# Kernel tuning notes

Hardware: AMD Instinct MI355X
Metric: run time of the kernel (lower is better)

## Reference

```python
import jax, jax.numpy as jnp
import numpy as np

INTER = 32  # inter_channels = in_channels // 2


def conv1x1(x, w, b):
    # x: (b, c_in, h, w), w: (c_out, c_in), b: (c_out,)
    return jnp.einsum('bchw,oc->bohw', x, w) + b[None, :, None, None]


def setup_inputs() -> dict:
    key = jax.random.key(0)
    ks = jax.random.split(key, 12)
    B, C, H, W = 8, 64, 64, 64
    inter = INTER
    s_in = 1.0 / np.sqrt(C)      # torch conv default init scale
    s_int = 1.0 / np.sqrt(inter)
    return {
        'x': jax.random.normal(ks[0], (B, C, H, W), jnp.float32),
        'g_w': jax.random.normal(ks[1], (inter, C), jnp.float32) * s_in,
        'g_b': jax.random.normal(ks[2], (inter,), jnp.float32) * s_in,
        'theta_w': jax.random.normal(ks[3], (inter, C), jnp.float32) * s_in,
        'theta_b': jax.random.normal(ks[4], (inter,), jnp.float32) * s_in,
        'phi_w': jax.random.normal(ks[5], (inter, C), jnp.float32) * s_in,
        'phi_b': jax.random.normal(ks[6], (inter,), jnp.float32) * s_in,
        'W_w': jax.random.normal(ks[7], (C, inter), jnp.float32) * s_int,
        'W_b': jax.random.normal(ks[8], (C,), jnp.float32) * s_int,
        'Wz1_w': jax.random.normal(ks[9], (C, inter), jnp.float32) * s_int,
        'Wz1_b': jax.random.normal(ks[10], (C,), jnp.float32) * s_int,
        'mb': jax.random.normal(ks[11], (inter, 256), jnp.float32),
    }


def reference(x, g_w, g_b, theta_w, theta_b, phi_w, phi_b, W_w, W_b, Wz1_w, Wz1_b, mb):
    b, c, h, w = x.shape
    inter = g_w.shape[0]
    # 1x1 conv projections, flattened over spatial: N = h*w
    g_x = conv1x1(x, g_w, g_b).reshape(b, inter, -1)          # (b, ic, N)
    theta_x = conv1x1(x, theta_w, theta_b).reshape(b, inter, -1)
    phi_x = conv1x1(x, phi_w, phi_b).reshape(b, inter, -1)    # (b, ic, N)
    # non-local self-attention: f = theta^T @ phi, unscaled softmax
    f = jnp.einsum('bcn,bcm->bnm', theta_x, phi_x)            # (b, N, N)
    f_div_C = jax.nn.softmax(f, axis=-1)
    y = jnp.einsum('bnm,bcm->bcn', f_div_C, g_x)              # (b, ic, N)
    y = y.reshape(b, inter, h, w)
    W_y = conv1x1(y, W_w, W_b)                                # (b, c, h, w)
    # memory-bank cross-attention: phi^T @ mb, scaled softmax
    f1 = jnp.einsum('bcn,ck->bnk', phi_x, mb)                 # (b, N, 256)
    scale = jnp.float32(int(inter) ** (-0.5))
    f_div_C1 = jax.nn.softmax(f1 * scale, axis=-1)
    y1 = jnp.einsum('bnk,ck->bcn', f_div_C1, mb)              # (b, ic, N)
    y1 = y1.reshape(b, inter, h, w)
    W_y1 = conv1x1(y1, Wz1_w, Wz1_b)
    return W_y + x + W_y1
```

## Files before the change

kernel.cpp:

```cpp
#include <hip/hip_runtime.h>
#include <hip/hip_bf16.h>

#define N_POS 4096
#define C_IN 64
#define IC 32
#define L2E 1.4426950408889634f

typedef float f32x16 __attribute__((ext_vector_type(16)));
typedef short bf16x8 __attribute__((ext_vector_type(8)));
typedef unsigned int uint;
typedef uint uint4v __attribute__((ext_vector_type(4)));
typedef unsigned short ushort;

static __device__ __forceinline__ ushort f2bf(float f) {
    __hip_bfloat16 h = __float2bfloat16(f);
    return __builtin_bit_cast(ushort, h);
}
static __device__ __forceinline__ float bf2f(ushort u) {
    uint v = ((uint)u) << 16;
    return __builtin_bit_cast(float, v);
}
static __device__ __forceinline__ uint packbf2(float lo, float hi) {
    return (uint)f2bf(lo) | ((uint)f2bf(hi) << 16);
}
static __device__ __forceinline__ uint packtrunc(float lo, float hi) {
    return __builtin_amdgcn_perm(__builtin_bit_cast(uint, hi),
                                 __builtin_bit_cast(uint, lo), 0x07060302u);
}

__global__ __launch_bounds__(128) void proj_kernel(
    const float* __restrict__ x,
    const float* __restrict__ g_w, const float* __restrict__ g_b,
    const float* __restrict__ th_w, const float* __restrict__ th_b,
    const float* __restrict__ ph_w, const float* __restrict__ ph_b,
    const float* __restrict__ mb,
    ushort* __restrict__ gcn, ushort* __restrict__ tht, ushort* __restrict__ pht,
    ushort* __restrict__ mbt, ushort* __restrict__ mbb)
{
    int gy = blockIdx.y;
    int pj = gy >> 1, half = gy & 1;
    const float* wsrc = (pj == 0) ? g_w : (pj == 1) ? th_w : ph_w;
    const float* bsrc = (pj == 0) ? g_b : (pj == 1) ? th_b : ph_b;
    __shared__ float w[16][64];
    __shared__ float bias[16];
    int tid = threadIdx.x;
    for (int i = tid; i < 1024; i += 128) w[i >> 6][i & 63] = wsrc[half * 1024 + i];
    if (tid < 16) bias[tid] = bsrc[half * 16 + tid];
    __syncthreads();

    int ng = blockIdx.x * 128 + tid;
    int b = ng >> 12, n = ng & 4095;
    const float* xb = x + (size_t)b * C_IN * N_POS + n;
    float xr[64];
    #pragma unroll
    for (int c = 0; c < 64; c++) xr[c] = xb[(size_t)c * N_POS];

    float acc[16];
    #pragma unroll
    for (int o = 0; o < 16; o++) {
        float a = bias[o];
        const float4* w4 = (const float4*)w[o];
        #pragma unroll
        for (int c4 = 0; c4 < 16; c4++) {
            float4 wv = w4[c4];
            a += wv.x * xr[c4*4+0] + wv.y * xr[c4*4+1]
               + wv.z * xr[c4*4+2] + wv.w * xr[c4*4+3];
        }
        if (pj == 1) a *= L2E;
        acc[o] = a;
    }

    if (pj == 0) {
        #pragma unroll
        for (int c = 0; c < 16; c++)
            gcn[((size_t)(b * IC + half * 16 + c)) * N_POS + n] = f2bf(acc[c]);
    } else {
        ushort* dst = ((pj == 1) ? tht : pht) + ((size_t)(b * N_POS + n)) * IC + half * 16;
        uint4v pk0, pk1;
        #pragma unroll
        for (int i = 0; i < 4; i++) pk0[i] = packbf2(acc[2*i], acc[2*i+1]);
        #pragma unroll
        for (int i = 0; i < 4; i++) pk1[i] = packbf2(acc[8+2*i], acc[8+2*i+1]);
        *(uint4v*)dst = pk0;
        *(uint4v*)(dst + 8) = pk1;
    }

    if (gy == 0 && blockIdx.x < 64) {
        int i = blockIdx.x * 128 + tid;
        int c = i >> 8, k = i & 255;
        float v = mb[i];
        mbb[i] = f2bf(v);
        mbt[k * 32 + c] = f2bf(v * (0.17677669529663687f * L2E));
    }
}

__global__ __launch_bounds__(256) void attn_kernel(
    const ushort* __restrict__ tht, const ushort* __restrict__ pht,
    const ushort* __restrict__ gcn, float* __restrict__ yp,
    float* __restrict__ dnm)
{
    __shared__ float redY[4][2][32][32];
    __shared__ float redD[4][2][32];
    int tid = threadIdx.x;
    int s = tid >> 6, lane = tid & 63;
    int bid = blockIdx.x;
    int b = bid & 7;
    int rest = bid >> 3;
    int qp = rest >> 1;
    int half = rest & 1;
    int q0 = qp * 64;
    int mbase = (half * 4 + s) * 512;
    int cl = lane & 31, h = lane >> 5;
    int t4 = (cl >> 2) & 3;
    int pcl = (t4 == 1 || t4 == 2) ? (cl ^ 12) : cl;

    const ushort* thpA = tht + ((size_t)(b * N_POS + q0 + cl)) * IC + 8 * h;
    bf16x8 thA0 = *(const bf16x8*)thpA;
    bf16x8 thA1 = *(const bf16x8*)(thpA + 16);
    const ushort* thpB = thpA + 32 * IC;
    bf16x8 thB0 = *(const bf16x8*)thpB;
    bf16x8 thB1 = *(const bf16x8*)(thpB + 16);

    const ushort* phbase = pht + (size_t)b * N_POS * IC;
    const ushort* gbase  = gcn + ((size_t)(b * IC + cl)) * N_POS;

    f32x16 yA0, yA1, yB0, yB1, zero;
    #pragma unroll
    for (int i = 0; i < 16; i++) {
        yA0[i] = 0.f; yA1[i] = 0.f; yB0[i] = 0.f; yB1[i] = 0.f; zero[i] = 0.f;
    }
    float sumeA = 0.f, sumeB = 0.f;

    #pragma unroll 2
    for (int mt = 0; mt < 16; ++mt) {
        int m0 = mbase + mt * 32;
        const ushort* php = phbase + ((size_t)(m0 + pcl)) * IC + 8 * h;
        bf16x8 ph0 = *(const bf16x8*)php;
        bf16x8 ph1 = *(const bf16x8*)(php + 16);
        const ushort* gp = gbase + m0 + 8 * h;
        bf16x8 g0 = *(const bf16x8*)gp;
        bf16x8 g1 = *(const bf16x8*)(gp + 16);

        f32x16 sv = __builtin_amdgcn_mfma_f32_32x32x16_bf16(ph0, thA0, zero, 0, 0, 0);
        sv = __builtin_amdgcn_mfma_f32_32x32x16_bf16(ph1, thA1, sv, 0, 0, 0);
        uint wA[8];
        #pragma unroll
        for (int i = 0; i < 8; i++) {
            float p0 = __builtin_amdgcn_exp2f(sv[2*i]);
            float p1 = __builtin_amdgcn_exp2f(sv[2*i+1]);
            sumeA += p0 + p1;
            wA[i] = packtrunc(p0, p1);
        }
        f32x16 sw = __builtin_amdgcn_mfma_f32_32x32x16_bf16(ph0, thB0, zero, 0, 0, 0);
        sw = __builtin_amdgcn_mfma_f32_32x32x16_bf16(ph1, thB1, sw, 0, 0, 0);
        uint wB[8];
        #pragma unroll
        for (int i = 0; i < 8; i++) {
            float p0 = __builtin_amdgcn_exp2f(sw[2*i]);
            float p1 = __builtin_amdgcn_exp2f(sw[2*i+1]);
            sumeB += p0 + p1;
            wB[i] = packtrunc(p0, p1);
        }

        uint4v aA0, aA1, aB0, aB1;
        aA0[0] = wA[0]; aA0[1] = wA[1]; aA0[2] = wA[2]; aA0[3] = wA[3];
        aA1[0] = wA[4]; aA1[1] = wA[5]; aA1[2] = wA[6]; aA1[3] = wA[7];
        aB0[0] = wB[0]; aB0[1] = wB[1]; aB0[2] = wB[2]; aB0[3] = wB[3];
        aB1[0] = wB[4]; aB1[1] = wB[5]; aB1[2] = wB[6]; aB1[3] = wB[7];

        yA0 = __builtin_amdgcn_mfma_f32_32x32x16_bf16(
            __builtin_bit_cast(bf16x8, aA0), g0, yA0, 0, 0, 0);
        yA1 = __builtin_amdgcn_mfma_f32_32x32x16_bf16(
            __builtin_bit_cast(bf16x8, aA1), g1, yA1, 0, 0, 0);
        yB0 = __builtin_amdgcn_mfma_f32_32x32x16_bf16(
            __builtin_bit_cast(bf16x8, aB0), g0, yB0, 0, 0, 0);
        yB1 = __builtin_amdgcn_mfma_f32_32x32x16_bf16(
            __builtin_bit_cast(bf16x8, aB1), g1, yB1, 0, 0, 0);
    }

    sumeA += __shfl_xor(sumeA, 32);
    sumeB += __shfl_xor(sumeB, 32);
    if (lane < 32) { redD[s][0][cl] = sumeA; redD[s][1][cl] = sumeB; }
    #pragma unroll
    for (int r = 0; r < 16; r++) {
        int q = (r & 3) + 8 * (r >> 2) + 4 * h;
        redY[s][0][q][cl] = yA0[r] + yA1[r];
        redY[s][1][q][cl] = yB0[r] + yB1[r];
    }
    __syncthreads();

    int q = tid >> 3, c4 = tid & 7;
    #pragma unroll
    for (int j = 0; j < 2; j++) {
        float den = redD[0][j][q] + redD[1][j][q] + redD[2][j][q] + redD[3][j][q];
        float4 v0 = *(const float4*)&redY[0][j][q][c4 * 4];
        float4 v1 = *(const float4*)&redY[1][j][q][c4 * 4];
        float4 v2 = *(const float4*)&redY[2][j][q][c4 * 4];
        float4 v3 = *(const float4*)&redY[3][j][q][c4 * 4];
        float4 vv;
        vv.x = v0.x + v1.x + v2.x + v3.x;
        vv.y = v0.y + v1.y + v2.y + v3.y;
        vv.z = v0.z + v1.z + v2.z + v3.z;
        vv.w = v0.w + v1.w + v2.w + v3.w;
        size_t t = ((size_t)(b * 128 + qp * 2 + j)) * 2 + half;
        *(float4*)(yp + t * 1024 + q * 32 + c4 * 4) = vv;
        if (c4 == 0) dnm[t * 32 + q] = den;
    }
}

__global__ __launch_bounds__(256) void mbout_kernel(
    const ushort* __restrict__ pht, const ushort* __restrict__ mbt,
    const ushort* __restrict__ mbb, const float* __restrict__ yp,
    const float* __restrict__ dnm, const float* __restrict__ x,
    const float* __restrict__ Ww, const float* __restrict__ Wb,
    const float* __restrict__ Wzw, const float* __restrict__ Wzb,
    float* __restrict__ out)
{
    __shared__ float sW[64][32], sWz[64][32];
    __shared__ float sb[64];
    __shared__ float ly1p[4][32][36];
    __shared__ float sumeL[4][32];
    int tid = threadIdx.x;
    int bid = blockIdx.x;
    int b = bid & 7, grp = bid >> 3;
    int n0 = grp * 64;

    for (int i = tid; i < 2048; i += 256) {
        sW[i >> 5][i & 31]  = Ww[i];
        sWz[i >> 5][i & 31] = Wzw[i];
    }
    if (tid < 64) sb[tid] = Wb[tid] + Wzb[tid];

    int s = tid >> 6, lane = tid & 63;
    int j = s & 1, kh = s >> 1;
    int q0 = n0 + j * 32;
    int cl = lane & 31, h = lane >> 5;
    int t4 = (cl >> 2) & 3;
    int pcl = (t4 == 1 || t4 == 2) ? (cl ^ 12) : cl;

    const ushort* php = pht + ((size_t)(b * N_POS + q0 + cl)) * IC + 8 * h;
    bf16x8 qf0 = *(const bf16x8*)php;
    bf16x8 qf1 = *(const bf16x8*)(php + 16);

    f32x16 yaccA, yaccB, zero;
    #pragma unroll
    for (int i = 0; i < 16; i++) { yaccA[i] = 0.f; yaccB[i] = 0.f; zero[i] = 0.f; }
    float sume = 0.f;

    #pragma unroll
    for (int kt = 0; kt < 4; ++kt) {
        int k0 = (kh * 4 + kt) * 32;
        const ushort* ap = mbt + ((size_t)(k0 + pcl)) * IC + 8 * h;
        bf16x8 af0 = *(const bf16x8*)ap;
        bf16x8 af1 = *(const bf16x8*)(ap + 16);
        const ushort* bp = mbb + (size_t)cl * 256 + k0 + 8 * h;
        bf16x8 bf0 = *(const bf16x8*)bp;
        bf16x8 bf1 = *(const bf16x8*)(bp + 16);

        f32x16 sv = __builtin_amdgcn_mfma_f32_32x32x16_bf16(af0, qf0, zero, 0, 0, 0);
        sv = __builtin_amdgcn_mfma_f32_32x32x16_bf16(af1, qf1, sv, 0, 0, 0);

        uint w[8];
        #pragma unroll
        for (int i = 0; i < 8; i++) {
            float p0 = __builtin_amdgcn_exp2f(sv[2*i]);
            float p1 = __builtin_amdgcn_exp2f(sv[2*i+1]);
            sume += p0 + p1;
            w[i] = packtrunc(p0, p1);
        }
        uint4v a0, a1;
        a0[0] = w[0]; a0[1] = w[1]; a0[2] = w[2]; a0[3] = w[3];
        a1[0] = w[4]; a1[1] = w[5]; a1[2] = w[6]; a1[3] = w[7];

        yaccA = __builtin_amdgcn_mfma_f32_32x32x16_bf16(
            __builtin_bit_cast(bf16x8, a0), bf0, yaccA, 0, 0, 0);
        yaccB = __builtin_amdgcn_mfma_f32_32x32x16_bf16(
            __builtin_bit_cast(bf16x8, a1), bf1, yaccB, 0, 0, 0);
    }

    sume += __shfl_xor(sume, 32);
    if (lane < 32) sumeL[s][cl] = sume;
    #pragma unroll
    for (int r = 0; r < 16; r++) {
        int q = (r & 3) + 8 * (r >> 2) + 4 * h;
        ly1p[s][q][cl] = yaccA[r] + yaccB[r];
    }
    __syncthreads();

    int obase = (s & 1) * 32 + (s >> 1) * 16;
    int n = n0 + lane;
    int jj = lane >> 5, q = lane & 31;

    float inv1 = 1.f / (sumeL[jj][q] + sumeL[2 + jj][q]);
    float y1v[32];
    #pragma unroll
    for (int c4 = 0; c4 < 8; c4++) {
        float4 p0 = *(const float4*)&ly1p[jj][q][c4 * 4];
        float4 p1 = *(const float4*)&ly1p[2 + jj][q][c4 * 4];
        y1v[c4*4+0] = (p0.x + p1.x) * inv1;
        y1v[c4*4+1] = (p0.y + p1.y) * inv1;
        y1v[c4*4+2] = (p0.z + p1.z) * inv1;
        y1v[c4*4+3] = (p0.w + p1.w) * inv1;
    }

    int qt = n >> 5;
    size_t t0 = ((size_t)(b * 128 + qt)) * 2;
    float inv = 1.f / (dnm[t0 * 32 + q] + dnm[t0 * 32 + 32 + q]);
    const float* yp0 = yp + t0 * 1024 + q * 32;
    const float* yp1 = yp0 + 1024;
    float yv[32];
    #pragma unroll
    for (int c4 = 0; c4 < 8; c4++) {
        float4 v0 = ((const float4*)yp0)[c4];
        float4 v1 = ((const float4*)yp1)[c4];
        yv[c4*4+0] = (v0.x + v1.x) * inv;
        yv[c4*4+1] = (v0.y + v1.y) * inv;
        yv[c4*4+2] = (v0.z + v1.z) * inv;
        yv[c4*4+3] = (v0.w + v1.w) * inv;
    }

    const float* xb = x   + ((size_t)(b * C_IN + obase)) * N_POS + n;
    float*       ob = out + ((size_t)(b * C_IN + obase)) * N_POS + n;
    for (int o = 0; o < 16; o++) {
        float acc = sb[obase + o] + xb[(size_t)o * N_POS];
        const float4* w4  = (const float4*)sW[obase + o];
        const float4* wz4 = (const float4*)sWz[obase + o];
        #pragma unroll
        for (int c4 = 0; c4 < 8; c4++) {
            float4 a = w4[c4], z = wz4[c4];
            acc += a.x * yv[c4*4+0] + a.y * yv[c4*4+1] + a.z * yv[c4*4+2] + a.w * yv[c4*4+3];
            acc += z.x * y1v[c4*4+0] + z.y * y1v[c4*4+1] + z.z * y1v[c4*4+2] + z.w * y1v[c4*4+3];
        }
        ob[(size_t)o * N_POS] = acc;
    }
}

extern "C" void kernel_launch(void* const* d_in, const int* in_sizes, int n_in,
                              void* d_out, int out_size, void* d_ws, size_t ws_size,
                              hipStream_t stream) {
    const float* x    = (const float*)d_in[0];
    const float* g_w  = (const float*)d_in[1];
    const float* g_b  = (const float*)d_in[2];
    const float* th_w = (const float*)d_in[3];
    const float* th_b = (const float*)d_in[4];
    const float* ph_w = (const float*)d_in[5];
    const float* ph_b = (const float*)d_in[6];
    const float* W_w  = (const float*)d_in[7];
    const float* W_b  = (const float*)d_in[8];
    const float* Wz_w = (const float*)d_in[9];
    const float* Wz_b = (const float*)d_in[10];
    const float* mb   = (const float*)d_in[11];
    float* out = (float*)d_out;

    char* w = (char*)d_ws;
    ushort* tht = (ushort*)w;
    ushort* pht = (ushort*)(w + (2u << 20));
    ushort* gcn = (ushort*)(w + (4u << 20));
    ushort* mbt = (ushort*)(w + (6u << 20));
    ushort* mbb = (ushort*)(w + (6u << 20) + 16384);
    float*  yp  = (float*)(w + (9u << 20));
    float*  dnm = (float*)(w + (17u << 20));

    proj_kernel<<<dim3(256, 6), 128, 0, stream>>>(x, g_w, g_b, th_w, th_b,
                                                  ph_w, ph_b, mb,
                                                  gcn, tht, pht, mbt, mbb);
    attn_kernel<<<1024, 256, 0, stream>>>(tht, pht, gcn, yp, dnm);
    mbout_kernel<<<512, 256, 0, stream>>>(pht, mbt, mbb, yp, dnm, x,
                                          W_w, W_b, Wz_w, Wz_b, out);
}
```

Baseline: 78.07 us.

## Fuse attention, memory-bank attention and output projection into one kernel

The separate attention and memory-bank/output kernels are merged into one 512-thread kernel. Each block now covers all 4096 keys for 64 queries using 8 waves, instead of two half-key blocks that wrote partial sums to global memory. After the attention loop, four waves compute the memory-bank attention while the other four add their partial outputs in shared memory. This removes the yp/dnm global round trip and one kernel launch. The cost is only 512 blocks with bigger blocks and more registers, and output weights are now read straight from global memory instead of being staged in shared memory.

```diff
diff --git a/kernel.cpp b/kernel.cpp
--- a/kernel.cpp
+++ b/kernel.cpp
@@ -15,10 +15,6 @@
 static __device__ __forceinline__ ushort f2bf(float f) {
     __hip_bfloat16 h = __float2bfloat16(f);
     return __builtin_bit_cast(ushort, h);
-}
-static __device__ __forceinline__ float bf2f(ushort u) {
-    uint v = ((uint)u) << 16;
-    return __builtin_bit_cast(float, v);
 }
 static __device__ __forceinline__ uint packbf2(float lo, float hi) {
     return (uint)f2bf(lo) | ((uint)f2bf(hi) << 16);
@@ -94,22 +90,26 @@
     }
 }
 
-__global__ __launch_bounds__(256) void attn_kernel(
+__global__ __launch_bounds__(512) void attn_fused(
     const ushort* __restrict__ tht, const ushort* __restrict__ pht,
-    const ushort* __restrict__ gcn, float* __restrict__ yp,
-    float* __restrict__ dnm)
+    const ushort* __restrict__ gcn, const ushort* __restrict__ mbt,
+    const ushort* __restrict__ mbb, const float* __restrict__ x,
+    const float* __restrict__ Ww, const float* __restrict__ Wb,
+    const float* __restrict__ Wzw, const float* __restrict__ Wzb,
+    float* __restrict__ out)
 {
-    __shared__ float redY[4][2][32][32];
-    __shared__ float redD[4][2][32];
+    __shared__ float redY[4][2][32][36];
+    __shared__ float redD[8][2][32];
+    __shared__ float ly1p[4][32][36];
+    __shared__ float sumeL[4][32];
+
     int tid = threadIdx.x;
     int s = tid >> 6, lane = tid & 63;
     int bid = blockIdx.x;
     int b = bid & 7;
-    int rest = bid >> 3;
-    int qp = rest >> 1;
-    int half = rest & 1;
+    int qp = bid >> 3;
     int q0 = qp * 64;
-    int mbase = (half * 4 + s) * 512;
+    int mbase = s * 512;
     int cl = lane & 31, h = lane >> 5;
     int t4 = (cl >> 2) & 3;
     int pcl = (t4 == 1 || t4 == 2) ? (cl ^ 12) : cl;
@@ -181,150 +181,114 @@
     sumeA += __shfl_xor(sumeA, 32);
     sumeB += __shfl_xor(sumeB, 32);
     if (lane < 32) { redD[s][0][cl] = sumeA; redD[s][1][cl] = sumeB; }
-    #pragma unroll
-    for (int r = 0; r < 16; r++) {
-        int q = (r & 3) + 8 * (r >> 2) + 4 * h;
-        redY[s][0][q][cl] = yA0[r] + yA1[r];
-        redY[s][1][q][cl] = yB0[r] + yB1[r];
+    if (s < 4) {
+        #pragma unroll
+        for (int r = 0; r < 16; r++) {
+            int q = (r & 3) + 8 * (r >> 2) + 4 * h;
+            redY[s][0][q][cl] = yA0[r] + yA1[r];
+            redY[s][1][q][cl] = yB0[r] + yB1[r];
+        }
     }
     __syncthreads();
 
-    int q = tid >> 3, c4 = tid & 7;
-    #pragma unroll
-    for (int j = 0; j < 2; j++) {
-        float den = redD[0][j][q] + redD[1][j][q] + redD[2][j][q] + redD[3][j][q];
-        float4 v0 = *(const float4*)&redY[0][j][q][c4 * 4];
-        float4 v1 = *(const float4*)&redY[1][j][q][c4 * 4];
-        float4 v2 = *(const float4*)&redY[2][j][q][c4 * 4];
-        float4 v3 = *(const float4*)&redY[3][j][q][c4 * 4];
-        float4 vv;
-        vv.x = v0.x + v1.x + v2.x + v3.x;
-        vv.y = v0.y + v1.y + v2.y + v3.y;
-        vv.z = v0.z + v1.z + v2.z + v3.z;
-        vv.w = v0.w + v1.w + v2.w + v3.w;
-        size_t t = ((size_t)(b * 128 + qp * 2 + j)) * 2 + half;
-        *(float4*)(yp + t * 1024 + q * 32 + c4 * 4) = vv;
-        if (c4 == 0) dnm[t * 32 + q] = den;
-    }
-}
-
-__global__ __launch_bounds__(256) void mbout_kernel(
-    const ushort* __restrict__ pht, const ushort* __restrict__ mbt,
-    const ushort* __restrict__ mbb, const float* __restrict__ yp,
-    const float* __restrict__ dnm, const float* __restrict__ x,
-    const float* __restrict__ Ww, const float* __restrict__ Wb,
-    const float* __restrict__ Wzw, const float* __restrict__ Wzb,
-    float* __restrict__ out)
-{
-    __shared__ float sW[64][32], sWz[64][32];
-    __shared__ float sb[64];
-    __shared__ float ly1p[4][32][36];
-    __shared__ float sumeL[4][32];
-    int tid = threadIdx.x;
-    int bid = blockIdx.x;
-    int b = bid & 7, grp = bid >> 3;
-    int n0 = grp * 64;
-
-    for (int i = tid; i < 2048; i += 256) {
-        sW[i >> 5][i & 31]  = Ww[i];
-        sWz[i >> 5][i & 31] = Wzw[i];
-    }
-    if (tid < 64) sb[tid] = Wb[tid] + Wzb[tid];
-
-    int s = tid >> 6, lane = tid & 63;
-    int j = s & 1, kh = s >> 1;
-    int q0 = n0 + j * 32;
-    int cl = lane & 31, h = lane >> 5;
-    int t4 = (cl >> 2) & 3;
-    int pcl = (t4 == 1 || t4 == 2) ? (cl ^ 12) : cl;
-
-    const ushort* php = pht + ((size_t)(b * N_POS + q0 + cl)) * IC + 8 * h;
-    bf16x8 qf0 = *(const bf16x8*)php;
-    bf16x8 qf1 = *(const bf16x8*)(php + 16);
-
-    f32x16 yaccA, yaccB, zero;
-    #pragma unroll
-    for (int i = 0; i < 16; i++) { yaccA[i] = 0.f; yaccB[i] = 0.f; zero[i] = 0.f; }
-    float sume = 0.f;
-
-    #pragma unroll
-    for (int kt = 0; kt < 4; ++kt) {
-        int k0 = (kh * 4 + kt) * 32;
-        const ushort* ap = mbt + ((size_t)(k0 + pcl)) * IC + 8 * h;
-        bf16x8 af0 = *(const bf16x8*)ap;
-        bf16x8 af1 = *(const bf16x8*)(ap + 16);
-        const ushort* bp = mbb + (size_t)cl * 256 + k0 + 8 * h;
-        bf16x8 bf0 = *(const bf16x8*)bp;
-        bf16x8 bf1 = *(const bf16x8*)(bp + 16);
-
-        f32x16 sv = __builtin_amdgcn_mfma_f32_32x32x16_bf16(af0, qf0, zero, 0, 0, 0);
-        sv = __builtin_amdgcn_mfma_f32_32x32x16_bf16(af1, qf1, sv, 0, 0, 0);
-
-        uint w[8];
-        #pragma unroll
-        for (int i = 0; i < 8; i++) {
-            float p0 = __builtin_amdgcn_exp2f(sv[2*i]);
-            float p1 = __builtin_amdgcn_exp2f(sv[2*i+1]);
-            sume += p0 + p1;
-            w[i] = packtrunc(p0, p1);
-        }
-        uint4v a0, a1;
-        a0[0] = w[0]; a0[1] = w[1]; a0[2] = w[2]; a0[3] = w[3];
-        a1[0] = w[4]; a1[1] = w[5]; a1[2] = w[6]; a1[3] = w[7];
-
-        yaccA = __builtin_amdgcn_mfma_f32_32x32x16_bf16(
-            __builtin_bit_cast(bf16x8, a0), bf0, yaccA, 0, 0, 0);
-        yaccB = __builtin_amdgcn_mfma_f32_32x32x16_bf16(
-            __builtin_bit_cast(bf16x8, a1), bf1, yaccB, 0, 0, 0);
-    }
-
-    sume += __shfl_xor(sume, 32);
-    if (lane < 32) sumeL[s][cl] = sume;
-    #pragma unroll
-    for (int r = 0; r < 16; r++) {
-        int q = (r & 3) + 8 * (r >> 2) + 4 * h;
-        ly1p[s][q][cl] = yaccA[r] + yaccB[r];
+    if (s >= 4) {
+        int sl = s - 4;
+        #pragma unroll
+        for (int r = 0; r < 16; r++) {
+            int q = (r & 3) + 8 * (r >> 2) + 4 * h;
+            redY[sl][0][q][cl] += yA0[r] + yA1[r];
+            redY[sl][1][q][cl] += yB0[r] + yB1[r];
+        }
+    } else {
+        int j = s & 1, kh = s >> 1;
+        int mq0 = q0 + j * 32;
+        const ushort* php = pht + ((size_t)(b * N_POS + mq0 + cl)) * IC + 8 * h;
+        bf16x8 qf0 = *(const bf16x8*)php;
+        bf16x8 qf1 = *(const bf16x8*)(php + 16);
+
+        f32x16 zA, zB;
+        #pragma unroll
+        for (int i = 0; i < 16; i++) { zA[i] = 0.f; zB[i] = 0.f; }
+        float sume = 0.f;
+
+        #pragma unroll
+        for (int kt = 0; kt < 4; ++kt) {
+            int k0 = (kh * 4 + kt) * 32;
+            const ushort* ap = mbt + ((size_t)(k0 + pcl)) * IC + 8 * h;
+            bf16x8 af0 = *(const bf16x8*)ap;
+            bf16x8 af1 = *(const bf16x8*)(ap + 16);
+            const ushort* bp = mbb + (size_t)cl * 256 + k0 + 8 * h;
+            bf16x8 bf0 = *(const bf16x8*)bp;
+            bf16x8 bf1 = *(const bf16x8*)(bp + 16);
+
+            f32x16 sv = __builtin_amdgcn_mfma_f32_32x32x16_bf16(af0, qf0, zero, 0, 0, 0);
+            sv = __builtin_amdgcn_mfma_f32_32x32x16_bf16(af1, qf1, sv, 0, 0, 0);
+
+            uint w[8];
+            #pragma unroll
+            for (int i = 0; i < 8; i++) {
+                float p0 = __builtin_amdgcn_exp2f(sv[2*i]);
+                float p1 = __builtin_amdgcn_exp2f(sv[2*i+1]);
+                sume += p0 + p1;
+                w[i] = packtrunc(p0, p1);
+            }
+            uint4v a0, a1;
+            a0[0] = w[0]; a0[1] = w[1]; a0[2] = w[2]; a0[3] = w[3];
+            a1[0] = w[4]; a1[1] = w[5]; a1[2] = w[6]; a1[3] = w[7];
+
+            zA = __builtin_amdgcn_mfma_f32_32x32x16_bf16(
+                __builtin_bit_cast(bf16x8, a0), bf0, zA, 0, 0, 0);
+            zB = __builtin_amdgcn_mfma_f32_32x32x16_bf16(
+                __builtin_bit_cast(bf16x8, a1), bf1, zB, 0, 0, 0);
+        }
+
+        sume += __shfl_xor(sume, 32);
+        if (lane < 32) sumeL[s][cl] = sume;
+        #pragma unroll
+        for (int r = 0; r < 16; r++) {
+            int q = (r & 3) + 8 * (r >> 2) + 4 * h;
+            ly1p[s][q][cl] = zA[r] + zB[r];
+        }
     }
     __syncthreads();
 
-    int obase = (s & 1) * 32 + (s >> 1) * 16;
-    int n = n0 + lane;
-    int jj = lane >> 5, q = lane & 31;
-
-    float inv1 = 1.f / (sumeL[jj][q] + sumeL[2 + jj][q]);
-    float y1v[32];
+    int nl = lane, og = s;
+    int n = q0 + nl;
+    int jo = nl >> 5, qo = nl & 31;
+
+    float den = 0.f;
+    #pragma unroll
+    for (int s8 = 0; s8 < 8; s8++) den += redD[s8][jo][qo];
+    float inv = 1.f / den;
+    float inv1 = 1.f / (sumeL[jo][qo] + sumeL[2 + jo][qo]);
+
+    float yv[32], y1v[32];
     #pragma unroll
     for (int c4 = 0; c4 < 8; c4++) {
-        float4 p0 = *(const float4*)&ly1p[jj][q][c4 * 4];
-        float4 p1 = *(const float4*)&ly1p[2 + jj][q][c4 * 4];
+        float4 v0 = *(const float4*)&redY[0][jo][qo][c4 * 4];
+        float4 v1 = *(const float4*)&redY[1][jo][qo][c4 * 4];
+        float4 v2 = *(const float4*)&redY[2][jo][qo][c4 * 4];
+        float4 v3 = *(const float4*)&redY[3][jo][qo][c4 * 4];
+        yv[c4*4+0] = (v0.x + v1.x + v2.x + v3.x) * inv;
+        yv[c4*4+1] = (v0.y + v1.y + v2.y + v3.y) * inv;
+        yv[c4*4+2] = (v0.z + v1.z + v2.z + v3.z) * inv;
+        yv[c4*4+3] = (v0.w + v1.w + v2.w + v3.w) * inv;
+        float4 p0 = *(const float4*)&ly1p[jo][qo][c4 * 4];
+        float4 p1 = *(const float4*)&ly1p[2 + jo][qo][c4 * 4];
         y1v[c4*4+0] = (p0.x + p1.x) * inv1;
         y1v[c4*4+1] = (p0.y + p1.y) * inv1;
         y1v[c4*4+2] = (p0.z + p1.z) * inv1;
         y1v[c4*4+3] = (p0.w + p1.w) * inv1;
     }
 
-    int qt = n >> 5;
-    size_t t0 = ((size_t)(b * 128 + qt)) * 2;
-    float inv = 1.f / (dnm[t0 * 32 + q] + dnm[t0 * 32 + 32 + q]);
-    const float* yp0 = yp + t0 * 1024 + q * 32;
-    const float* yp1 = yp0 + 1024;
-    float yv[32];
-    #pragma unroll
-    for (int c4 = 0; c4 < 8; c4++) {
-        float4 v0 = ((const float4*)yp0)[c4];
-        float4 v1 = ((const float4*)yp1)[c4];
-        yv[c4*4+0] = (v0.x + v1.x) * inv;
-        yv[c4*4+1] = (v0.y + v1.y) * inv;
-        yv[c4*4+2] = (v0.z + v1.z) * inv;
-        yv[c4*4+3] = (v0.w + v1.w) * inv;
-    }
-
+    int obase = og * 8;
     const float* xb = x   + ((size_t)(b * C_IN + obase)) * N_POS + n;
     float*       ob = out + ((size_t)(b * C_IN + obase)) * N_POS + n;
-    for (int o = 0; o < 16; o++) {
-        float acc = sb[obase + o] + xb[(size_t)o * N_POS];
-        const float4* w4  = (const float4*)sW[obase + o];
-        const float4* wz4 = (const float4*)sWz[obase + o];
+    #pragma unroll
+    for (int o = 0; o < 8; o++) {
+        float acc = Wb[obase + o] + Wzb[obase + o] + xb[(size_t)o * N_POS];
+        const float4* w4  = (const float4*)(Ww  + (obase + o) * 32);
+        const float4* wz4 = (const float4*)(Wzw + (obase + o) * 32);
         #pragma unroll
         for (int c4 = 0; c4 < 8; c4++) {
             float4 a = w4[c4], z = wz4[c4];
@@ -358,13 +322,10 @@
     ushort* gcn = (ushort*)(w + (4u << 20));
     ushort* mbt = (ushort*)(w + (6u << 20));
     ushort* mbb = (ushort*)(w + (6u << 20) + 16384);
-    float*  yp  = (float*)(w + (9u << 20));
-    float*  dnm = (float*)(w + (17u << 20));
 
     proj_kernel<<<dim3(256, 6), 128, 0, stream>>>(x, g_w, g_b, th_w, th_b,
                                                   ph_w, ph_b, mb,
                                                   gcn, tht, pht, mbt, mbb);
-    attn_kernel<<<1024, 256, 0, stream>>>(tht, pht, gcn, yp, dnm);
-    mbout_kernel<<<512, 256, 0, stream>>>(pht, mbt, mbb, yp, dnm, x,
-                                          W_w, W_b, Wz_w, Wz_b, out);
-}
+    attn_fused<<<512, 512, 0, stream>>>(tht, pht, gcn, mbt, mbb, x,
+                                        W_w, W_b, Wz_w, Wz_b, out);
+}
```

After: 74.31 us. -4.8%, faster.

## Widen attention query tile to 128 and split projection into quarter-channel blocks

Applied to the files above, without the earlier changes.

The attention kernel now gives each block 128 queries (four 32-row tiles) instead of 64. Each loaded phi/g tile is reused across four query tiles, and the grid drops to 512 blocks. The cross-wave reduction now goes through a padded shared buffer with two-stage accumulation, and the partial-sum layout in yp/dnm changes to match, with the consumer kernel updated accordingly. Separately, the projection kernel is split into 12 y-blocks of 8 output channels each, raising parallelism at the cost of re-reading x more times. The wider tile raises register pressure (four accumulators plus eight theta fragments) and halves the number of attention blocks, which may hurt occupancy.

```diff
diff --git a/kernel.cpp b/kernel.cpp
--- a/kernel.cpp
+++ b/kernel.cpp
@@ -15,10 +15,6 @@
 static __device__ __forceinline__ ushort f2bf(float f) {
     __hip_bfloat16 h = __float2bfloat16(f);
     return __builtin_bit_cast(ushort, h);
-}
-static __device__ __forceinline__ float bf2f(ushort u) {
-    uint v = ((uint)u) << 16;
-    return __builtin_bit_cast(float, v);
 }
 static __device__ __forceinline__ uint packbf2(float lo, float hi) {
     return (uint)f2bf(lo) | ((uint)f2bf(hi) << 16);
@@ -38,14 +34,14 @@
     ushort* __restrict__ mbt, ushort* __restrict__ mbb)
 {
     int gy = blockIdx.y;
-    int pj = gy >> 1, half = gy & 1;
+    int pj = gy >> 2, q8 = gy & 3;
     const float* wsrc = (pj == 0) ? g_w : (pj == 1) ? th_w : ph_w;
     const float* bsrc = (pj == 0) ? g_b : (pj == 1) ? th_b : ph_b;
-    __shared__ float w[16][64];
-    __shared__ float bias[16];
+    __shared__ float w[8][64];
+    __shared__ float bias[8];
     int tid = threadIdx.x;
-    for (int i = tid; i < 1024; i += 128) w[i >> 6][i & 63] = wsrc[half * 1024 + i];
-    if (tid < 16) bias[tid] = bsrc[half * 16 + tid];
+    for (int i = tid; i < 512; i += 128) w[i >> 6][i & 63] = wsrc[q8 * 512 + i];
+    if (tid < 8) bias[tid] = bsrc[q8 * 8 + tid];
     __syncthreads();
 
     int ng = blockIdx.x * 128 + tid;
@@ -55,9 +51,9 @@
     #pragma unroll
     for (int c = 0; c < 64; c++) xr[c] = xb[(size_t)c * N_POS];
 
-    float acc[16];
-    #pragma unroll
-    for (int o = 0; o < 16; o++) {
+    float acc[8];
+    #pragma unroll
+    for (int o = 0; o < 8; o++) {
         float a = bias[o];
         const float4* w4 = (const float4*)w[o];
         #pragma unroll
@@ -72,17 +68,14 @@
 
     if (pj == 0) {
         #pragma unroll
-        for (int c = 0; c < 16; c++)
-            gcn[((size_t)(b * IC + half * 16 + c)) * N_POS + n] = f2bf(acc[c]);
+        for (int c = 0; c < 8; c++)
+            gcn[((size_t)(b * IC + q8 * 8 + c)) * N_POS + n] = f2bf(acc[c]);
     } else {
-        ushort* dst = ((pj == 1) ? tht : pht) + ((size_t)(b * N_POS + n)) * IC + half * 16;
-        uint4v pk0, pk1;
-        #pragma unroll
-        for (int i = 0; i < 4; i++) pk0[i] = packbf2(acc[2*i], acc[2*i+1]);
-        #pragma unroll
-        for (int i = 0; i < 4; i++) pk1[i] = packbf2(acc[8+2*i], acc[8+2*i+1]);
-        *(uint4v*)dst = pk0;
-        *(uint4v*)(dst + 8) = pk1;
+        ushort* dst = ((pj == 1) ? tht : pht) + ((size_t)(b * N_POS + n)) * IC + q8 * 8;
+        uint4v pk;
+        #pragma unroll
+        for (int i = 0; i < 4; i++) pk[i] = packbf2(acc[2*i], acc[2*i+1]);
+        *(uint4v*)dst = pk;
     }
 
     if (gy == 0 && blockIdx.x < 64) {
@@ -99,37 +92,60 @@
     const ushort* __restrict__ gcn, float* __restrict__ yp,
     float* __restrict__ dnm)
 {
-    __shared__ float redY[4][2][32][32];
-    __shared__ float redD[4][2][32];
+    __shared__ float redY[2][4][32][36];
+    __shared__ float redD[4][4][32];
     int tid = threadIdx.x;
     int s = tid >> 6, lane = tid & 63;
     int bid = blockIdx.x;
     int b = bid & 7;
     int rest = bid >> 3;
-    int qp = rest >> 1;
-    int half = rest & 1;
-    int q0 = qp * 64;
-    int mbase = (half * 4 + s) * 512;
+    int qq = rest >> 1;
+    int mh = rest & 1;
+    int q0 = qq * 128;
+    int mbase = (mh * 4 + s) * 512;
     int cl = lane & 31, h = lane >> 5;
     int t4 = (cl >> 2) & 3;
     int pcl = (t4 == 1 || t4 == 2) ? (cl ^ 12) : cl;
 
-    const ushort* thpA = tht + ((size_t)(b * N_POS + q0 + cl)) * IC + 8 * h;
-    bf16x8 thA0 = *(const bf16x8*)thpA;
-    bf16x8 thA1 = *(const bf16x8*)(thpA + 16);
-    const ushort* thpB = thpA + 32 * IC;
-    bf16x8 thB0 = *(const bf16x8*)thpB;
-    bf16x8 thB1 = *(const bf16x8*)(thpB + 16);
+    const ushort* thp = tht + ((size_t)(b * N_POS + q0 + cl)) * IC + 8 * h;
+    bf16x8 th00 = *(const bf16x8*)thp;
+    bf16x8 th01 = *(const bf16x8*)(thp + 16);
+    bf16x8 th10 = *(const bf16x8*)(thp + 32 * IC);
+    bf16x8 th11 = *(const bf16x8*)(thp + 32 * IC + 16);
+    bf16x8 th20 = *(const bf16x8*)(thp + 64 * IC);
+    bf16x8 th21 = *(const bf16x8*)(thp + 64 * IC + 16);
+    bf16x8 th30 = *(const bf16x8*)(thp + 96 * IC);
+    bf16x8 th31 = *(const bf16x8*)(thp + 96 * IC + 16);
 
     const ushort* phbase = pht + (size_t)b * N_POS * IC;
     const ushort* gbase  = gcn + ((size_t)(b * IC + cl)) * N_POS;
 
-    f32x16 yA0, yA1, yB0, yB1, zero;
+    f32x16 y0, y1a, y2, y3, zero;
     #pragma unroll
     for (int i = 0; i < 16; i++) {
-        yA0[i] = 0.f; yA1[i] = 0.f; yB0[i] = 0.f; yB1[i] = 0.f; zero[i] = 0.f;
-    }
-    float sumeA = 0.f, sumeB = 0.f;
+        y0[i] = 0.f; y1a[i] = 0.f; y2[i] = 0.f; y3[i] = 0.f; zero[i] = 0.f;
+    }
+    float su0 = 0.f, su1 = 0.f, su2 = 0.f, su3 = 0.f;
+
+#define QTILE(T0, T1, SU, Y) do {                                              \
+        f32x16 sv = __builtin_amdgcn_mfma_f32_32x32x16_bf16(ph0, T0, zero, 0, 0, 0); \
+        sv = __builtin_amdgcn_mfma_f32_32x32x16_bf16(ph1, T1, sv, 0, 0, 0);    \
+        uint w_[8];                                                            \
+        _Pragma("unroll")                                                      \
+        for (int i_ = 0; i_ < 8; i_++) {                                       \
+            float p0_ = __builtin_amdgcn_exp2f(sv[2*i_]);                      \
+            float p1_ = __builtin_amdgcn_exp2f(sv[2*i_+1]);                    \
+            SU += p0_ + p1_;                                                   \
+            w_[i_] = packtrunc(p0_, p1_);                                      \
+        }                                                                      \
+        uint4v a0_, a1_;                                                       \
+        a0_[0] = w_[0]; a0_[1] = w_[1]; a0_[2] = w_[2]; a0_[3] = w_[3];        \
+        a1_[0] = w_[4]; a1_[1] = w_[5]; a1_[2] = w_[6]; a1_[3] = w_[7];        \
+        Y = __builtin_amdgcn_mfma_f32_32x32x16_bf16(                           \
+            __builtin_bit_cast(bf16x8, a0_), g0, Y, 0, 0, 0);                  \
+        Y = __builtin_amdgcn_mfma_f32_32x32x16_bf16(                           \
+            __builtin_bit_cast(bf16x8, a1_), g1, Y, 0, 0, 0);                  \
+    } while (0)
 
     #pragma unroll 2
     for (int mt = 0; mt < 16; ++mt) {
@@ -141,70 +157,55 @@
         bf16x8 g0 = *(const bf16x8*)gp;
         bf16x8 g1 = *(const bf16x8*)(gp + 16);
 
-        f32x16 sv = __builtin_amdgcn_mfma_f32_32x32x16_bf16(ph0, thA0, zero, 0, 0, 0);
-        sv = __builtin_amdgcn_mfma_f32_32x32x16_bf16(ph1, thA1, sv, 0, 0, 0);
-        uint wA[8];
-        #pragma unroll
-        for (int i = 0; i < 8; i++) {
-            float p0 = __builtin_amdgcn_exp2f(sv[2*i]);
-            float p1 = __builtin_amdgcn_exp2f(sv[2*i+1]);
-            sumeA += p0 + p1;
-            wA[i] = packtrunc(p0, p1);
-        }
-        f32x16 sw = __builtin_amdgcn_mfma_f32_32x32x16_bf16(ph0, thB0, zero, 0, 0, 0);
-        sw = __builtin_amdgcn_mfma_f32_32x32x16_bf16(ph1, thB1, sw, 0, 0, 0);
-        uint wB[8];
-        #pragma unroll
-        for (int i = 0; i < 8; i++) {
-            float p0 = __builtin_amdgcn_exp2f(sw[2*i]);
-            float p1 = __builtin_amdgcn_exp2f(sw[2*i+1]);
-            sumeB += p0 + p1;
-            wB[i] = packtrunc(p0, p1);
-        }
-
-        uint4v aA0, aA1, aB0, aB1;
-        aA0[0] = wA[0]; aA0[1] = wA[1]; aA0[2] = wA[2]; aA0[3] = wA[3];
-        aA1[0] = wA[4]; aA1[1] = wA[5]; aA1[2] = wA[6]; aA1[3] = wA[7];
-        aB0[0] = wB[0]; aB0[1] = wB[1]; aB0[2] = wB[2]; aB0[3] = wB[3];
-        aB1[0] = wB[4]; aB1[1] = wB[5]; aB1[2] = wB[6]; aB1[3] = wB[7];
-
-        yA0 = __builtin_amdgcn_mfma_f32_32x32x16_bf16(
-            __builtin_bit_cast(bf16x8, aA0), g0, yA0, 0, 0, 0);
-        yA1 = __builtin_amdgcn_mfma_f32_32x32x16_bf16(
-            __builtin_bit_cast(bf16x8, aA1), g1, yA1, 0, 0, 0);
-        yB0 = __builtin_amdgcn_mfma_f32_32x32x16_bf16(
-            __builtin_bit_cast(bf16x8, aB0), g0, yB0, 0, 0, 0);
-        yB1 = __builtin_amdgcn_mfma_f32_32x32x16_bf16(
-            __builtin_bit_cast(bf16x8, aB1), g1, yB1, 0, 0, 0);
-    }
-
-    sumeA += __shfl_xor(sumeA, 32);
-    sumeB += __shfl_xor(sumeB, 32);
-    if (lane < 32) { redD[s][0][cl] = sumeA; redD[s][1][cl] = sumeB; }
-    #pragma unroll
-    for (int r = 0; r < 16; r++) {
-        int q = (r & 3) + 8 * (r >> 2) + 4 * h;
-        redY[s][0][q][cl] = yA0[r] + yA1[r];
-        redY[s][1][q][cl] = yB0[r] + yB1[r];
+        QTILE(th00, th01, su0, y0);
+        QTILE(th10, th11, su1, y1a);
+        QTILE(th20, th21, su2, y2);
+        QTILE(th30, th31, su3, y3);
+    }
+#undef QTILE
+
+    su0 += __shfl_xor(su0, 32);
+    su1 += __shfl_xor(su1, 32);
+    su2 += __shfl_xor(su2, 32);
+    su3 += __shfl_xor(su3, 32);
+    if (lane < 32) {
+        redD[s][0][cl] = su0; redD[s][1][cl] = su1;
+        redD[s][2][cl] = su2; redD[s][3][cl] = su3;
+    }
+
+    if (s >= 2) {
+        #pragma unroll
+        for (int r = 0; r < 16; r++) {
+            int q = (r & 3) + 8 * (r >> 2) + 4 * h;
+            redY[s - 2][0][q][cl] = y0[r];
+            redY[s - 2][1][q][cl] = y1a[r];
+            redY[s - 2][2][q][cl] = y2[r];
+            redY[s - 2][3][q][cl] = y3[r];
+        }
     }
     __syncthreads();
-
-    int q = tid >> 3, c4 = tid & 7;
-    #pragma unroll
-    for (int j = 0; j < 2; j++) {
-        float den = redD[0][j][q] + redD[1][j][q] + redD[2][j][q] + redD[3][j][q];
-        float4 v0 = *(const float4*)&redY[0][j][q][c4 * 4];
-        float4 v1 = *(const float4*)&redY[1][j][q][c4 * 4];
-        float4 v2 = *(const float4*)&redY[2][j][q][c4 * 4];
-        float4 v3 = *(const float4*)&redY[3][j][q][c4 * 4];
-        float4 vv;
-        vv.x = v0.x + v1.x + v2.x + v3.x;
-        vv.y = v0.y + v1.y + v2.y + v3.y;
-        vv.z = v0.z + v1.z + v2.z + v3.z;
-        vv.w = v0.w + v1.w + v2.w + v3.w;
-        size_t t = ((size_t)(b * 128 + qp * 2 + j)) * 2 + half;
-        *(float4*)(yp + t * 1024 + q * 32 + c4 * 4) = vv;
-        if (c4 == 0) dnm[t * 32 + q] = den;
+    if (s < 2) {
+        #pragma unroll
+        for (int r = 0; r < 16; r++) {
+            int q = (r & 3) + 8 * (r >> 2) + 4 * h;
+            redY[s][0][q][cl] += y0[r];
+            redY[s][1][q][cl] += y1a[r];
+            redY[s][2][q][cl] += y2[r];
+            redY[s][3][q][cl] += y3[r];
+        }
+    }
+    __syncthreads();
+
+    size_t pbase = ((size_t)((b * 32 + qq) * 2 + mh)) * 4096;
+    for (int i = tid; i < 4096; i += 256) {
+        int t = i >> 10, rm = i & 1023;
+        int q = rm >> 5, c = rm & 31;
+        yp[pbase + i] = redY[0][t][q][c] + redY[1][t][q][c];
+    }
+    if (tid < 128) {
+        int t = tid >> 5, q = tid & 31;
+        dnm[((size_t)((b * 32 + qq) * 2 + mh)) * 128 + tid] =
+            redD[0][t][q] + redD[1][t][q] + redD[2][t][q] + redD[3][t][q];
     }
 }
 
@@ -304,10 +305,13 @@
     }
 
     int qt = n >> 5;
-    size_t t0 = ((size_t)(b * 128 + qt)) * 2;
-    float inv = 1.f / (dnm[t0 * 32 + q] + dnm[t0 * 32 + 32 + q]);
-    const float* yp0 = yp + t0 * 1024 + q * 32;
-    const float* yp1 = yp0 + 1024;
+    int qqn = qt >> 2, tt = qt & 3;
+    size_t pb = ((size_t)((b * 32 + qqn) * 2)) * 4096;
+    size_t db = ((size_t)((b * 32 + qqn) * 2)) * 128;
+    float den = dnm[db + tt * 32 + q] + dnm[db + 128 + tt * 32 + q];
+    float inv = 1.f / den;
+    const float* yp0 = yp + pb + tt * 1024 + q * 32;
+    const float* yp1 = yp0 + 4096;
     float yv[32];
     #pragma unroll
     for (int c4 = 0; c4 < 8; c4++) {
@@ -361,10 +365,10 @@
     float*  yp  = (float*)(w + (9u << 20));
     float*  dnm = (float*)(w + (17u << 20));
 
-    proj_kernel<<<dim3(256, 6), 128, 0, stream>>>(x, g_w, g_b, th_w, th_b,
-                                                  ph_w, ph_b, mb,
-                                                  gcn, tht, pht, mbt, mbb);
-    attn_kernel<<<1024, 256, 0, stream>>>(tht, pht, gcn, yp, dnm);
+    proj_kernel<<<dim3(256, 12), 128, 0, stream>>>(x, g_w, g_b, th_w, th_b,
+                                                   ph_w, ph_b, mb,
+                                                   gcn, tht, pht, mbt, mbb);
+    attn_kernel<<<512, 256, 0, stream>>>(tht, pht, gcn, yp, dnm);
     mbout_kernel<<<512, 256, 0, stream>>>(pht, mbt, mbb, yp, dnm, x,
                                           W_w, W_b, Wz_w, Wz_b, out);
 }
```

New measurement: 80.22 us. 1.03x slower.
